# Kernel optimization log

Hardware: AMD Instinct MI355X
Metric: run time of the kernel (lower is better)

Reference implementation:

```python
import jax, jax.numpy as jnp
import numpy as np

B, T, D_IN = 2, 2048, 1024
H, D_HEAD = 16, 64
D_INNER = H * D_HEAD  # 1024
D_OUT = D_HEAD        # out_proj maps d_inner -> d_out


def setup_inputs() -> dict:
    key = jax.random.key(0)
    ks = jax.random.split(key, 6)
    s_in = 1.0 / np.sqrt(D_IN)
    s_inner = 1.0 / np.sqrt(D_INNER)
    return {
        "x": jax.random.normal(ks[0], (B, T, D_IN), dtype=jnp.float32),
        "Wq": jax.random.uniform(ks[1], (D_IN, D_INNER), jnp.float32, -s_in, s_in),
        "Wk": jax.random.uniform(ks[2], (D_IN, D_INNER), jnp.float32, -s_in, s_in),
        "Wv": jax.random.uniform(ks[3], (D_IN, D_INNER), jnp.float32, -s_in, s_in),
        "Wo": jax.random.uniform(ks[4], (D_INNER, D_OUT), jnp.float32, -s_inner, s_inner),
        "bo": jax.random.uniform(ks[5], (D_OUT,), jnp.float32, -s_inner, s_inner),
    }


def reference(x, Wq, Wk, Wv, Wo, bo):
    b, t, _ = x.shape
    # projections -> [b, h, t, d]
    def split_heads(y):
        return y.reshape(b, t, H, D_HEAD).transpose(0, 2, 1, 3)
    q = split_heads(x @ Wq)
    k = split_heads(x @ Wk)
    v = split_heads(x @ Wv)
    scores = jnp.einsum("bhqd,bhkd->bhqk", q, k)
    causal = jnp.triu(jnp.ones((t, t), dtype=bool), k=1)
    scores = jnp.where(causal, -jnp.inf, scores)
    # NOTE: original scales by sqrt(d_out*num_heads), not sqrt(head_dim)
    attn = jax.nn.softmax(scores / np.sqrt(D_INNER), axis=-1)
    y = jnp.einsum("bhqk,bhkd->bhqd", attn, v)
    y = y.transpose(0, 2, 1, 3).reshape(b, t, D_INNER)
    return y @ Wo + bo
```

## Files before the change

### kernel.cpp

```cpp
#include <hip/hip_runtime.h>

typedef __attribute__((ext_vector_type(8))) short short8;
typedef __attribute__((ext_vector_type(4))) float f32x4;
typedef __attribute__((ext_vector_type(8))) unsigned short ushort8v;


__device__ __forceinline__ unsigned short f2bf(float f) {
  union { float f; unsigned int u; } x; x.f = f;
  unsigned int r = x.u + 0x7FFFu + ((x.u >> 16) & 1u);
  return (unsigned short)(r >> 16);
}

__device__ __forceinline__ void gload_lds16(const void* g, void* l) {
  __builtin_amdgcn_global_load_lds(
      (const __attribute__((address_space(1))) void*)g,
      (__attribute__((address_space(3))) void*)l, 16, 0, 0);
}


__global__ __launch_bounds__(256) void prep(
    const float* __restrict__ x,
    const float* __restrict__ Wq, const float* __restrict__ Wk, const float* __restrict__ Wv,
    const float* __restrict__ Wo, const float* __restrict__ bo,
    unsigned short* __restrict__ xb,
    unsigned short* __restrict__ wqt, unsigned short* __restrict__ wkt,
    unsigned short* __restrict__ wvt, unsigned short* __restrict__ wot,
    float* __restrict__ out) {
  __shared__ float tile[32][33];
  int b = blockIdx.x;
  if (b < 4096) {
    int i = (b * 256 + threadIdx.x) * 4;
    float4 f = *(const float4*)(x + i);
    ushort4 o;
    o.x = f2bf(f.x); o.y = f2bf(f.y); o.z = f2bf(f.z); o.w = f2bf(f.w);
    *(ushort4*)(xb + i) = o;
  } else if (b < 7168) {
    int idx = b - 4096;
    int z = idx >> 10, rem = idx & 1023;
    const float* src = (z == 0) ? Wq : (z == 1) ? Wk : Wv;
    unsigned short* dst = (z == 0) ? wqt : (z == 1) ? wkt : wvt;
    int kx = (rem & 31) * 32, ny = (rem >> 5) * 32;
    int tx = threadIdx.x & 31, ty = threadIdx.x >> 5;
    #pragma unroll
    for (int r = 0; r < 32; r += 8)
      tile[ty + r][tx] = src[(size_t)(kx + ty + r) * 1024 + ny + tx];
    __syncthreads();
    #pragma unroll
    for (int r = 0; r < 32; r += 8)
      dst[(size_t)(ny + ty + r) * 1024 + kx + tx] = f2bf(tile[tx][ty + r]);
  } else if (b < 7232) {
    int idx = b - 7168;
    int kx = (idx & 31) * 32, ny = (idx >> 5) * 32;
    int tx = threadIdx.x & 31, ty = threadIdx.x >> 5;
    #pragma unroll
    for (int r = 0; r < 32; r += 8)
      tile[ty + r][tx] = Wo[(size_t)(kx + ty + r) * 64 + ny + tx];
    __syncthreads();
    #pragma unroll
    for (int r = 0; r < 32; r += 8)
      wot[(size_t)(ny + ty + r) * 1024 + kx + tx] = f2bf(tile[tx][ty + r]);
  } else {
    int t = (b - 7232) * 256 + threadIdx.x;
    float4 bi = *(const float4*)(bo + (t & 15) * 4);
    *(float4*)(out + (size_t)t * 4) = bi;
  }
}


__global__ __launch_bounds__(256) void qkv_gemm(
    const unsigned short* __restrict__ Xb,
    const unsigned short* __restrict__ Wqt, const unsigned short* __restrict__ Wkt,
    const unsigned short* __restrict__ Wvt,
    unsigned short* __restrict__ Oq, unsigned short* __restrict__ Ok,
    unsigned short* __restrict__ Ovt) {
  constexpr int Kd = 1024;
  __shared__ __align__(16) unsigned short As[128 * 64];
  __shared__ __align__(16) unsigned short Bs[128 * 64];
  int z = blockIdx.z;
  int m0, n0;
  const unsigned short *Arow, *Brow;
  if (z == 2) {
    m0 = blockIdx.x * 128; n0 = blockIdx.y * 128;
    Arow = Xb; Brow = Wvt;
  } else {
    m0 = blockIdx.y * 128; n0 = blockIdx.x * 128;
    Arow = (z == 0) ? Wqt : Wkt; Brow = Xb;
  }
  int tid = threadIdx.x, lane = tid & 63, wave = tid >> 6;
  int wm = wave >> 1, wn = wave & 1;
  int l15 = lane & 15, quad = lane >> 4;
  int swz = l15 & 7;

  f32x4 acc[4][4] = {};

  for (int k0 = 0; k0 < Kd; k0 += 64) {
    __syncthreads();
    #pragma unroll
    for (int r = 0; r < 4; ++r) {
      int i = tid + 256 * r;
      int row = i >> 3, c8 = i & 7;
      int gc8 = c8 ^ (row & 7);
      gload_lds16(Arow + (size_t)(m0 + row) * Kd + k0 + gc8 * 8, &As[i * 8]);
    }
    #pragma unroll
    for (int r = 0; r < 4; ++r) {
      int i = tid + 256 * r;
      int row = i >> 3, c8 = i & 7;
      int gc8 = c8 ^ (row & 7);
      gload_lds16(Brow + (size_t)(n0 + row) * Kd + k0 + gc8 * 8, &Bs[i * 8]);
    }
    __syncthreads();
    short8 af[4][2], bf[4][2];
    #pragma unroll
    for (int s = 0; s < 2; ++s) {
      #pragma unroll
      for (int i = 0; i < 4; ++i)
        af[i][s] = *(const short8*)&As[(wm * 64 + i * 16 + l15) * 64 + (((s << 2) + quad) ^ swz) * 8];
      #pragma unroll
      for (int j = 0; j < 4; ++j)
        bf[j][s] = *(const short8*)&Bs[(wn * 64 + j * 16 + l15) * 64 + (((s << 2) + quad) ^ swz) * 8];
    }
    #pragma unroll
    for (int s = 0; s < 2; ++s)
      #pragma unroll
      for (int i = 0; i < 4; ++i)
        #pragma unroll
        for (int j = 0; j < 4; ++j)
          acc[i][j] = __builtin_amdgcn_mfma_f32_16x16x32_bf16(af[i][s], bf[j][s], acc[i][j], 0, 0, 0);
  }

  if (z == 2) {
    #pragma unroll
    for (int i = 0; i < 4; ++i) {
      int tbase = m0 + wm * 64 + i * 16 + quad * 4;
      int b = tbase >> 11, tt = tbase & 2047;
      #pragma unroll
      for (int j = 0; j < 4; ++j) {
        int dm = n0 + wn * 64 + j * 16 + l15;
        int h = dm >> 6, d = dm & 63;
        unsigned int u0 = f2bf(acc[i][j][0]), u1 = f2bf(acc[i][j][1]);
        unsigned int u2 = f2bf(acc[i][j][2]), u3 = f2bf(acc[i][j][3]);
        uint2 pk; pk.x = u0 | (u1 << 16); pk.y = u2 | (u3 << 16);
        *(uint2*)(Ovt + (((size_t)(b * 16 + h) * 64 + d) << 11) + tt) = pk;
      }
    }
  } else {
    unsigned short* O = (z == 0) ? Oq : Ok;
    float scale = (z == 0) ? 0.0450842200f : 1.0f;
    #pragma unroll
    for (int i = 0; i < 4; ++i) {
      int dmbase = m0 + wm * 64 + i * 16 + quad * 4;
      int h = dmbase >> 6, d0 = dmbase & 63;
      #pragma unroll
      for (int j = 0; j < 4; ++j) {
        int t = n0 + wn * 64 + j * 16 + l15;
        int b = t >> 11, tt = t & 2047;
        unsigned int u0 = f2bf(acc[i][j][0] * scale), u1 = f2bf(acc[i][j][1] * scale);
        unsigned int u2 = f2bf(acc[i][j][2] * scale), u3 = f2bf(acc[i][j][3] * scale);
        uint2 pk; pk.x = u0 | (u1 << 16); pk.y = u2 | (u3 << 16);
        *(uint2*)(O + (((size_t)(b * 16 + h) * 2048 + tt) << 6) + d0) = pk;
      }
    }
  }
}


__global__ __launch_bounds__(256, 2) void attn10(
    const unsigned short* __restrict__ Qg, const unsigned short* __restrict__ Kg,
    const unsigned short* __restrict__ Vtg, unsigned short* __restrict__ Yg) {
  constexpr int T = 2048;
  __shared__ __align__(16) unsigned short Ks[2][64 * 64];
  __shared__ __align__(16) unsigned short Vs[2][64 * 64];
  __shared__ __align__(16) unsigned short Ps[4][32 * 64];
  int bh = blockIdx.x;
  int by = blockIdx.y;
  int pp = (by < 8) ? by : 23 - by;
  int qtA = pp, qtB = 31 - pp;
  int tid = threadIdx.x, lane = tid & 63, wave = tid >> 6;
  int l15 = lane & 15, quad = lane >> 4;
  int swz = l15 & 7;
  const unsigned short* Qb = Qg + (size_t)bh * T * 64;
  const unsigned short* Kb = Kg + (size_t)bh * T * 64;
  const unsigned short* Vb = Vtg + (size_t)bh * 64 * T;
  int h = bh & 15, b = bh >> 4;
  int qw[2] = {qtA * 64 + wave * 16, qtB * 64 + wave * 16};

  short8 qf[2][2];
  #pragma unroll
  for (int jq = 0; jq < 2; ++jq)
    #pragma unroll
    for (int s = 0; s < 2; ++s)
      qf[jq][s] = *(const short8*)(Qb + (size_t)(qw[jq] + l15) * 64 + quad * 8 + 32 * s);

  f32x4 Oacc[2][4] = {};
  float m_run[2] = {-__builtin_inff(), -__builtin_inff()};
  float l_run[2] = {0.f, 0.f};

  int srow = tid >> 3, sc8 = tid & 7;
  int sdst = srow * 64 + ((sc8 ^ (srow & 7)) * 8);

  ushort8v kpre[2], vpre[2];
  #pragma unroll
  for (int r = 0; r < 2; ++r) {
    kpre[r] = *(const ushort8v*)(Kb + (size_t)(srow + 32 * r) * 64 + sc8 * 8);
    vpre[r] = *(const ushort8v*)(Vb + (size_t)(srow + 32 * r) * T + sc8 * 8);
  }
  *(ushort8v*)&Ks[0][sdst] = kpre[0];
  *(ushort8v*)&Ks[0][sdst + 2048] = kpre[1];
  *(ushort8v*)&Vs[0][sdst] = vpre[0];
  *(ushort8v*)&Vs[0][sdst + 2048] = vpre[1];
  __syncthreads();

  for (int kt = 0; kt <= qtA; ++kt) {
    const unsigned short* Kl = Ks[kt & 1];
    const unsigned short* Vl = Vs[kt & 1];
    unsigned short* Kn = Ks[(kt & 1) ^ 1];
    unsigned short* Vn = Vs[(kt & 1) ^ 1];

    #pragma unroll
    for (int r = 0; r < 2; ++r) {
      kpre[r] = *(const ushort8v*)(Kb + (size_t)((kt + 1) * 64 + srow + 32 * r) * 64 + sc8 * 8);
      vpre[r] = *(const ushort8v*)(Vb + (size_t)(srow + 32 * r) * T + (kt + 1) * 64 + sc8 * 8);
    }

    f32x4 S[4][2] = {};
    __builtin_amdgcn_s_setprio(1);
    #pragma unroll
    for (int s = 0; s < 2; ++s)
      #pragma unroll
      for (int mi = 0; mi < 4; ++mi) {
        short8 kf = *(const short8*)&Kl[(mi * 16 + l15) * 64 + ((quad + 4 * s) ^ swz) * 8];
        #pragma unroll
        for (int jq = 0; jq < 2; ++jq)
          S[mi][jq] = __builtin_amdgcn_mfma_f32_16x16x32_bf16(kf, qf[jq][s], S[mi][jq], 0, 0, 0);
      }
    __builtin_amdgcn_s_setprio(0);

    if (kt == qtA) {
      int ql = wave * 16 + l15;
      #pragma unroll
      for (int mi = 0; mi < 4; ++mi) {
        int tokl = mi * 16 + quad * 4;
        #pragma unroll
        for (int r = 0; r < 4; ++r)
          if (tokl + r > ql) S[mi][0][r] = -__builtin_inff();
      }
    }

    float alpha[2]; bool norescale[2];
    #pragma unroll
    for (int jq = 0; jq < 2; ++jq) {
      float t0 = fmaxf(fmaxf(S[0][jq][0], S[0][jq][1]), fmaxf(S[0][jq][2], S[0][jq][3]));
      float t1 = fmaxf(fmaxf(S[1][jq][0], S[1][jq][1]), fmaxf(S[1][jq][2], S[1][jq][3]));
      float t2 = fmaxf(fmaxf(S[2][jq][0], S[2][jq][1]), fmaxf(S[2][jq][2], S[2][jq][3]));
      float t3 = fmaxf(fmaxf(S[3][jq][0], S[3][jq][1]), fmaxf(S[3][jq][2], S[3][jq][3]));
      float vmax = fmaxf(fmaxf(t0, t1), fmaxf(t2, t3));
      vmax = fmaxf(vmax, __shfl_xor(vmax, 16));
      vmax = fmaxf(vmax, __shfl_xor(vmax, 32));
      float mold = m_run[jq];
      bool defer = __all(vmax - mold <= 8.f) != 0;
      float mnew = defer ? mold : fmaxf(mold, vmax);
      alpha[jq] = defer ? 1.f : __builtin_amdgcn_exp2f(mold - mnew);
      norescale[jq] = defer;
      m_run[jq] = mnew;
      float rs = 0.f;
      #pragma unroll
      for (int mi = 0; mi < 4; ++mi) {
        float p0 = __builtin_amdgcn_exp2f(S[mi][jq][0] - mnew);
        float p1 = __builtin_amdgcn_exp2f(S[mi][jq][1] - mnew);
        float p2 = __builtin_amdgcn_exp2f(S[mi][jq][2] - mnew);
        float p3 = __builtin_amdgcn_exp2f(S[mi][jq][3] - mnew);
        rs += (p0 + p1) + (p2 + p3);
        union { float f; unsigned int u; } a0{p0}, a1{p1}, a2{p2}, a3{p3};
        uint2 pk;
        pk.x = ((a0.u + 0x8000u) >> 16) | ((a1.u + 0x8000u) & 0xFFFF0000u);
        pk.y = ((a2.u + 0x8000u) >> 16) | ((a3.u + 0x8000u) & 0xFFFF0000u);
        int g = (2 * mi + (quad >> 1)) ^ swz;
        *(uint2*)&Ps[wave][(jq * 16 + l15) * 64 + g * 8 + (quad & 1) * 4] = pk;
      }
      rs += __shfl_xor(rs, 16);
      rs += __shfl_xor(rs, 32);
      l_run[jq] = l_run[jq] * alpha[jq] + rs;
    }

    #pragma unroll
    for (int jq = 0; jq < 2; ++jq)
      if (!norescale[jq])
        #pragma unroll
        for (int jd = 0; jd < 4; ++jd)
          #pragma unroll
          for (int r = 0; r < 4; ++r)
            Oacc[jq][jd][r] *= alpha[jq];

    *(ushort8v*)&Kn[sdst] = kpre[0];
    *(ushort8v*)&Kn[sdst + 2048] = kpre[1];
    *(ushort8v*)&Vn[sdst] = vpre[0];
    *(ushort8v*)&Vn[sdst + 2048] = vpre[1];

    __builtin_amdgcn_s_setprio(1);
    #pragma unroll
    for (int s = 0; s < 2; ++s) {
      short8 vfr[4];
      #pragma unroll
      for (int jd = 0; jd < 4; ++jd)
        vfr[jd] = *(const short8*)&Vl[(jd * 16 + l15) * 64 + ((quad + 4 * s) ^ swz) * 8];
      #pragma unroll
      for (int jq = 0; jq < 2; ++jq) {
        short8 pf = *(const short8*)&Ps[wave][(jq * 16 + l15) * 64 + ((quad + 4 * s) ^ swz) * 8];
        #pragma unroll
        for (int jd = 0; jd < 4; ++jd)
          Oacc[jq][jd] = __builtin_amdgcn_mfma_f32_16x16x32_bf16(vfr[jd], pf, Oacc[jq][jd], 0, 0, 0);
      }
    }
    __builtin_amdgcn_s_setprio(0);
    __syncthreads();
  }

  for (int kt = qtA + 1; kt <= qtB; ++kt) {
    const unsigned short* Kl = Ks[kt & 1];
    const unsigned short* Vl = Vs[kt & 1];
    unsigned short* Kn = Ks[(kt & 1) ^ 1];
    unsigned short* Vn = Vs[(kt & 1) ^ 1];

    if (kt < qtB) {
      #pragma unroll
      for (int r = 0; r < 2; ++r) {
        kpre[r] = *(const ushort8v*)(Kb + (size_t)((kt + 1) * 64 + srow + 32 * r) * 64 + sc8 * 8);
        vpre[r] = *(const ushort8v*)(Vb + (size_t)(srow + 32 * r) * T + (kt + 1) * 64 + sc8 * 8);
      }
    }

    f32x4 S[4] = {};
    __builtin_amdgcn_s_setprio(1);
    #pragma unroll
    for (int s = 0; s < 2; ++s)
      #pragma unroll
      for (int mi = 0; mi < 4; ++mi) {
        short8 kf = *(const short8*)&Kl[(mi * 16 + l15) * 64 + ((quad + 4 * s) ^ swz) * 8];
        S[mi] = __builtin_amdgcn_mfma_f32_16x16x32_bf16(kf, qf[1][s], S[mi], 0, 0, 0);
      }
    __builtin_amdgcn_s_setprio(0);

    if (kt == qtB) {
      int ql = wave * 16 + l15;
      #pragma unroll
      for (int mi = 0; mi < 4; ++mi) {
        int tokl = mi * 16 + quad * 4;
        #pragma unroll
        for (int r = 0; r < 4; ++r)
          if (tokl + r > ql) S[mi][r] = -__builtin_inff();
      }
    }

    float t0 = fmaxf(fmaxf(S[0][0], S[0][1]), fmaxf(S[0][2], S[0][3]));
    float t1 = fmaxf(fmaxf(S[1][0], S[1][1]), fmaxf(S[1][2], S[1][3]));
    float t2 = fmaxf(fmaxf(S[2][0], S[2][1]), fmaxf(S[2][2], S[2][3]));
    float t3 = fmaxf(fmaxf(S[3][0], S[3][1]), fmaxf(S[3][2], S[3][3]));
    float vmax = fmaxf(fmaxf(t0, t1), fmaxf(t2, t3));
    vmax = fmaxf(vmax, __shfl_xor(vmax, 16));
    vmax = fmaxf(vmax, __shfl_xor(vmax, 32));
    float mold = m_run[1];
    bool defer = __all(vmax - mold <= 8.f) != 0;
    float mnew = defer ? mold : fmaxf(mold, vmax);
    float alpha = defer ? 1.f : __builtin_amdgcn_exp2f(mold - mnew);
    m_run[1] = mnew;
    float rs = 0.f;
    #pragma unroll
    for (int mi = 0; mi < 4; ++mi) {
      float p0 = __builtin_amdgcn_exp2f(S[mi][0] - mnew);
      float p1 = __builtin_amdgcn_exp2f(S[mi][1] - mnew);
      float p2 = __builtin_amdgcn_exp2f(S[mi][2] - mnew);
      float p3 = __builtin_amdgcn_exp2f(S[mi][3] - mnew);
      rs += (p0 + p1) + (p2 + p3);
      union { float f; unsigned int u; } a0{p0}, a1{p1}, a2{p2}, a3{p3};
      uint2 pk;
      pk.x = ((a0.u + 0x8000u) >> 16) | ((a1.u + 0x8000u) & 0xFFFF0000u);
      pk.y = ((a2.u + 0x8000u) >> 16) | ((a3.u + 0x8000u) & 0xFFFF0000u);
      int g = (2 * mi + (quad >> 1)) ^ swz;
      *(uint2*)&Ps[wave][(16 + l15) * 64 + g * 8 + (quad & 1) * 4] = pk;
    }
    rs += __shfl_xor(rs, 16);
    rs += __shfl_xor(rs, 32);
    l_run[1] = l_run[1] * alpha + rs;

    if (!defer)
      #pragma unroll
      for (int jd = 0; jd < 4; ++jd)
        #pragma unroll
        for (int r = 0; r < 4; ++r)
          Oacc[1][jd][r] *= alpha;

    if (kt < qtB) {
      *(ushort8v*)&Kn[sdst] = kpre[0];
      *(ushort8v*)&Kn[sdst + 2048] = kpre[1];
      *(ushort8v*)&Vn[sdst] = vpre[0];
      *(ushort8v*)&Vn[sdst + 2048] = vpre[1];
    }

    __builtin_amdgcn_s_setprio(1);
    #pragma unroll
    for (int s = 0; s < 2; ++s) {
      short8 pf = *(const short8*)&Ps[wave][(16 + l15) * 64 + ((quad + 4 * s) ^ swz) * 8];
      #pragma unroll
      for (int jd = 0; jd < 4; ++jd) {
        short8 vfr = *(const short8*)&Vl[(jd * 16 + l15) * 64 + ((quad + 4 * s) ^ swz) * 8];
        Oacc[1][jd] = __builtin_amdgcn_mfma_f32_16x16x32_bf16(vfr, pf, Oacc[1][jd], 0, 0, 0);
      }
    }
    __builtin_amdgcn_s_setprio(0);
    __syncthreads();
  }

  #pragma unroll
  for (int jq = 0; jq < 2; ++jq) {
    float linv = 1.f / l_run[jq];
    int q = qw[jq] + l15;
    size_t row = (size_t)(b * 2048 + q) * 1024 + h * 64 + quad * 4;
    #pragma unroll
    for (int jd = 0; jd < 4; ++jd) {
      unsigned int u0 = f2bf(Oacc[jq][jd][0] * linv), u1 = f2bf(Oacc[jq][jd][1] * linv);
      unsigned int u2 = f2bf(Oacc[jq][jd][2] * linv), u3 = f2bf(Oacc[jq][jd][3] * linv);
      uint2 pk; pk.x = u0 | (u1 << 16); pk.y = u2 | (u3 << 16);
      *(uint2*)(Yg + row + jd * 16) = pk;
    }
  }
}


__global__ __launch_bounds__(256) void oproj(
    const unsigned short* __restrict__ Y, const unsigned short* __restrict__ Wot,
    float* __restrict__ out) {
  __shared__ __align__(16) unsigned short As[64 * 32];
  __shared__ __align__(16) unsigned short Bs[64 * 32];
  int m0 = blockIdx.x * 64;
  int kbase = blockIdx.y * 256;
  int tid = threadIdx.x, lane = tid & 63, wave = tid >> 6;
  int l15 = lane & 15, quad = lane >> 4;
  f32x4 acc[4] = {};
  for (int k0 = kbase; k0 < kbase + 256; k0 += 32) {
    __syncthreads();
    {
      int row = tid >> 2, c8 = (tid & 3) * 8;
      gload_lds16(Y + (size_t)(m0 + row) * 1024 + k0 + c8, &As[tid * 8]);
      gload_lds16(Wot + (size_t)row * 1024 + k0 + c8, &Bs[tid * 8]);
    }
    __syncthreads();
    short8 af = *(const short8*)&As[(wave * 16 + l15) * 32 + quad * 8];
    #pragma unroll
    for (int j = 0; j < 4; ++j) {
      short8 bf = *(const short8*)&Bs[(j * 16 + l15) * 32 + quad * 8];
      acc[j] = __builtin_amdgcn_mfma_f32_16x16x32_bf16(af, bf, acc[j], 0, 0, 0);
    }
  }
  #pragma unroll
  for (int j = 0; j < 4; ++j) {
    int n = j * 16 + l15;
    #pragma unroll
    for (int r = 0; r < 4; ++r) {
      int m = m0 + wave * 16 + quad * 4 + r;
      atomicAdd(&out[(size_t)m * 64 + n], acc[j][r]);
    }
  }
}


extern "C" void kernel_launch(void* const* d_in, const int* in_sizes, int n_in,
                              void* d_out, int out_size, void* d_ws, size_t ws_size,
                              hipStream_t stream) {
  const float* x  = (const float*)d_in[0];
  const float* Wq = (const float*)d_in[1];
  const float* Wk = (const float*)d_in[2];
  const float* Wv = (const float*)d_in[3];
  const float* Wo = (const float*)d_in[4];
  const float* bo = (const float*)d_in[5];
  float* out = (float*)d_out;
  char* ws = (char*)d_ws;

  unsigned short* xb  = (unsigned short*)(ws);
  unsigned short* wqt = (unsigned short*)(ws + (8ull << 20));
  unsigned short* wkt = (unsigned short*)(ws + (10ull << 20));
  unsigned short* wvt = (unsigned short*)(ws + (12ull << 20));
  unsigned short* wot = (unsigned short*)(ws + (14ull << 20));
  unsigned short* q   = (unsigned short*)(ws + (15ull << 20));
  unsigned short* k   = (unsigned short*)(ws + (23ull << 20));
  unsigned short* vt  = (unsigned short*)(ws + (31ull << 20));
  unsigned short* y   = (unsigned short*)(ws + (39ull << 20));

  prep<<<7488, 256, 0, stream>>>(x, Wq, Wk, Wv, Wo, bo, xb, wqt, wkt, wvt, wot, out);
  qkv_gemm<<<dim3(32, 8, 3), 256, 0, stream>>>(xb, wqt, wkt, wvt, q, k, vt);
  attn10<<<dim3(32, 16), 256, 0, stream>>>(q, k, vt, y);
  oproj<<<dim3(64, 4), 256, 0, stream>>>(y, wot, out);
}
```

Baseline: 163.0 us.

## Split paired causal query tiles into one tile per block for higher occupancy

The attention kernel no longer gives each block two query tiles (a short and a long one paired for causal balance). Each block now handles a single 64-row query tile, so the grid doubles to 32x32 blocks. Blocks are ordered so short and long tiles interleave, and the P staging buffer is halved. This cuts registers and shared memory per block so launch bounds can request 4 blocks per CU instead of 2, and the final barrier is skipped. The cost is that K/V tiles for the low-index key ranges are loaded by more blocks, and per-block work becomes uneven, which now relies on the scheduler to balance it.

```diff
diff --git a/kernel.cpp b/kernel.cpp
--- a/kernel.cpp
+++ b/kernel.cpp
@@ -165,17 +165,17 @@
 }
 
 
-__global__ __launch_bounds__(256, 2) void attn10(
+__global__ __launch_bounds__(256, 4) void attn11(
     const unsigned short* __restrict__ Qg, const unsigned short* __restrict__ Kg,
     const unsigned short* __restrict__ Vtg, unsigned short* __restrict__ Yg) {
   constexpr int T = 2048;
   __shared__ __align__(16) unsigned short Ks[2][64 * 64];
   __shared__ __align__(16) unsigned short Vs[2][64 * 64];
-  __shared__ __align__(16) unsigned short Ps[4][32 * 64];
+  __shared__ __align__(16) unsigned short Ps[4][16 * 64];
   int bh = blockIdx.x;
   int by = blockIdx.y;
-  int pp = (by < 8) ? by : 23 - by;
-  int qtA = pp, qtB = 31 - pp;
+  int g = by >> 3, w8 = by & 7;
+  int qt = (g == 0) ? w8 : (g == 1) ? (15 - w8) : (g == 2) ? (16 + w8) : (31 - w8);
   int tid = threadIdx.x, lane = tid & 63, wave = tid >> 6;
   int l15 = lane & 15, quad = lane >> 4;
   int swz = l15 & 7;
@@ -183,18 +183,16 @@
   const unsigned short* Kb = Kg + (size_t)bh * T * 64;
   const unsigned short* Vb = Vtg + (size_t)bh * 64 * T;
   int h = bh & 15, b = bh >> 4;
-  int qw[2] = {qtA * 64 + wave * 16, qtB * 64 + wave * 16};
-
-  short8 qf[2][2];
+  int qw = qt * 64 + wave * 16;
+
+  short8 qf[2];
   #pragma unroll
-  for (int jq = 0; jq < 2; ++jq)
-    #pragma unroll
-    for (int s = 0; s < 2; ++s)
-      qf[jq][s] = *(const short8*)(Qb + (size_t)(qw[jq] + l15) * 64 + quad * 8 + 32 * s);
-
-  f32x4 Oacc[2][4] = {};
-  float m_run[2] = {-__builtin_inff(), -__builtin_inff()};
-  float l_run[2] = {0.f, 0.f};
+  for (int s = 0; s < 2; ++s)
+    qf[s] = *(const short8*)(Qb + (size_t)(qw + l15) * 64 + quad * 8 + 32 * s);
+
+  f32x4 Oacc[4] = {};
+  float m_run = -__builtin_inff();
+  float l_run = 0.f;
 
   int srow = tid >> 3, sc8 = tid & 7;
   int sdst = srow * 64 + ((sc8 ^ (srow & 7)) * 8);
@@ -211,118 +209,13 @@
   *(ushort8v*)&Vs[0][sdst + 2048] = vpre[1];
   __syncthreads();
 
-  for (int kt = 0; kt <= qtA; ++kt) {
+  for (int kt = 0; kt <= qt; ++kt) {
     const unsigned short* Kl = Ks[kt & 1];
     const unsigned short* Vl = Vs[kt & 1];
     unsigned short* Kn = Ks[(kt & 1) ^ 1];
     unsigned short* Vn = Vs[(kt & 1) ^ 1];
 
-    #pragma unroll
-    for (int r = 0; r < 2; ++r) {
-      kpre[r] = *(const ushort8v*)(Kb + (size_t)((kt + 1) * 64 + srow + 32 * r) * 64 + sc8 * 8);
-      vpre[r] = *(const ushort8v*)(Vb + (size_t)(srow + 32 * r) * T + (kt + 1) * 64 + sc8 * 8);
-    }
-
-    f32x4 S[4][2] = {};
-    __builtin_amdgcn_s_setprio(1);
-    #pragma unroll
-    for (int s = 0; s < 2; ++s)
-      #pragma unroll
-      for (int mi = 0; mi < 4; ++mi) {
-        short8 kf = *(const short8*)&Kl[(mi * 16 + l15) * 64 + ((quad + 4 * s) ^ swz) * 8];
-        #pragma unroll
-        for (int jq = 0; jq < 2; ++jq)
-          S[mi][jq] = __builtin_amdgcn_mfma_f32_16x16x32_bf16(kf, qf[jq][s], S[mi][jq], 0, 0, 0);
-      }
-    __builtin_amdgcn_s_setprio(0);
-
-    if (kt == qtA) {
-      int ql = wave * 16 + l15;
-      #pragma unroll
-      for (int mi = 0; mi < 4; ++mi) {
-        int tokl = mi * 16 + quad * 4;
-        #pragma unroll
-        for (int r = 0; r < 4; ++r)
-          if (tokl + r > ql) S[mi][0][r] = -__builtin_inff();
-      }
-    }
-
-    float alpha[2]; bool norescale[2];
-    #pragma unroll
-    for (int jq = 0; jq < 2; ++jq) {
-      float t0 = fmaxf(fmaxf(S[0][jq][0], S[0][jq][1]), fmaxf(S[0][jq][2], S[0][jq][3]));
-      float t1 = fmaxf(fmaxf(S[1][jq][0], S[1][jq][1]), fmaxf(S[1][jq][2], S[1][jq][3]));
-      float t2 = fmaxf(fmaxf(S[2][jq][0], S[2][jq][1]), fmaxf(S[2][jq][2], S[2][jq][3]));
-      float t3 = fmaxf(fmaxf(S[3][jq][0], S[3][jq][1]), fmaxf(S[3][jq][2], S[3][jq][3]));
-      float vmax = fmaxf(fmaxf(t0, t1), fmaxf(t2, t3));
-      vmax = fmaxf(vmax, __shfl_xor(vmax, 16));
-      vmax = fmaxf(vmax, __shfl_xor(vmax, 32));
-      float mold = m_run[jq];
-      bool defer = __all(vmax - mold <= 8.f) != 0;
-      float mnew = defer ? mold : fmaxf(mold, vmax);
-      alpha[jq] = defer ? 1.f : __builtin_amdgcn_exp2f(mold - mnew);
-      norescale[jq] = defer;
-      m_run[jq] = mnew;
-      float rs = 0.f;
-      #pragma unroll
-      for (int mi = 0; mi < 4; ++mi) {
-        float p0 = __builtin_amdgcn_exp2f(S[mi][jq][0] - mnew);
-        float p1 = __builtin_amdgcn_exp2f(S[mi][jq][1] - mnew);
-        float p2 = __builtin_amdgcn_exp2f(S[mi][jq][2] - mnew);
-        float p3 = __builtin_amdgcn_exp2f(S[mi][jq][3] - mnew);
-        rs += (p0 + p1) + (p2 + p3);
-        union { float f; unsigned int u; } a0{p0}, a1{p1}, a2{p2}, a3{p3};
-        uint2 pk;
-        pk.x = ((a0.u + 0x8000u) >> 16) | ((a1.u + 0x8000u) & 0xFFFF0000u);
-        pk.y = ((a2.u + 0x8000u) >> 16) | ((a3.u + 0x8000u) & 0xFFFF0000u);
-        int g = (2 * mi + (quad >> 1)) ^ swz;
-        *(uint2*)&Ps[wave][(jq * 16 + l15) * 64 + g * 8 + (quad & 1) * 4] = pk;
-      }
-      rs += __shfl_xor(rs, 16);
-      rs += __shfl_xor(rs, 32);
-      l_run[jq] = l_run[jq] * alpha[jq] + rs;
-    }
-
-    #pragma unroll
-    for (int jq = 0; jq < 2; ++jq)
-      if (!norescale[jq])
-        #pragma unroll
-        for (int jd = 0; jd < 4; ++jd)
-          #pragma unroll
-          for (int r = 0; r < 4; ++r)
-            Oacc[jq][jd][r] *= alpha[jq];
-
-    *(ushort8v*)&Kn[sdst] = kpre[0];
-    *(ushort8v*)&Kn[sdst + 2048] = kpre[1];
-    *(ushort8v*)&Vn[sdst] = vpre[0];
-    *(ushort8v*)&Vn[sdst + 2048] = vpre[1];
-
-    __builtin_amdgcn_s_setprio(1);
-    #pragma unroll
-    for (int s = 0; s < 2; ++s) {
-      short8 vfr[4];
-      #pragma unroll
-      for (int jd = 0; jd < 4; ++jd)
-        vfr[jd] = *(const short8*)&Vl[(jd * 16 + l15) * 64 + ((quad + 4 * s) ^ swz) * 8];
-      #pragma unroll
-      for (int jq = 0; jq < 2; ++jq) {
-        short8 pf = *(const short8*)&Ps[wave][(jq * 16 + l15) * 64 + ((quad + 4 * s) ^ swz) * 8];
-        #pragma unroll
-        for (int jd = 0; jd < 4; ++jd)
-          Oacc[jq][jd] = __builtin_amdgcn_mfma_f32_16x16x32_bf16(vfr[jd], pf, Oacc[jq][jd], 0, 0, 0);
-      }
-    }
-    __builtin_amdgcn_s_setprio(0);
-    __syncthreads();
-  }
-
-  for (int kt = qtA + 1; kt <= qtB; ++kt) {
-    const unsigned short* Kl = Ks[kt & 1];
-    const unsigned short* Vl = Vs[kt & 1];
-    unsigned short* Kn = Ks[(kt & 1) ^ 1];
-    unsigned short* Vn = Vs[(kt & 1) ^ 1];
-
-    if (kt < qtB) {
+    if (kt < qt) {
       #pragma unroll
       for (int r = 0; r < 2; ++r) {
         kpre[r] = *(const ushort8v*)(Kb + (size_t)((kt + 1) * 64 + srow + 32 * r) * 64 + sc8 * 8);
@@ -337,11 +230,11 @@
       #pragma unroll
       for (int mi = 0; mi < 4; ++mi) {
         short8 kf = *(const short8*)&Kl[(mi * 16 + l15) * 64 + ((quad + 4 * s) ^ swz) * 8];
-        S[mi] = __builtin_amdgcn_mfma_f32_16x16x32_bf16(kf, qf[1][s], S[mi], 0, 0, 0);
+        S[mi] = __builtin_amdgcn_mfma_f32_16x16x32_bf16(kf, qf[s], S[mi], 0, 0, 0);
       }
     __builtin_amdgcn_s_setprio(0);
 
-    if (kt == qtB) {
+    if (kt == qt) {
       int ql = wave * 16 + l15;
       #pragma unroll
       for (int mi = 0; mi < 4; ++mi) {
@@ -359,11 +252,11 @@
     float vmax = fmaxf(fmaxf(t0, t1), fmaxf(t2, t3));
     vmax = fmaxf(vmax, __shfl_xor(vmax, 16));
     vmax = fmaxf(vmax, __shfl_xor(vmax, 32));
-    float mold = m_run[1];
+    float mold = m_run;
     bool defer = __all(vmax - mold <= 8.f) != 0;
     float mnew = defer ? mold : fmaxf(mold, vmax);
     float alpha = defer ? 1.f : __builtin_amdgcn_exp2f(mold - mnew);
-    m_run[1] = mnew;
+    m_run = mnew;
     float rs = 0.f;
     #pragma unroll
     for (int mi = 0; mi < 4; ++mi) {
@@ -376,21 +269,21 @@
       uint2 pk;
       pk.x = ((a0.u + 0x8000u) >> 16) | ((a1.u + 0x8000u) & 0xFFFF0000u);
       pk.y = ((a2.u + 0x8000u) >> 16) | ((a3.u + 0x8000u) & 0xFFFF0000u);
-      int g = (2 * mi + (quad >> 1)) ^ swz;
-      *(uint2*)&Ps[wave][(16 + l15) * 64 + g * 8 + (quad & 1) * 4] = pk;
+      int gg = (2 * mi + (quad >> 1)) ^ swz;
+      *(uint2*)&Ps[wave][l15 * 64 + gg * 8 + (quad & 1) * 4] = pk;
     }
     rs += __shfl_xor(rs, 16);
     rs += __shfl_xor(rs, 32);
-    l_run[1] = l_run[1] * alpha + rs;
+    l_run = l_run * alpha + rs;
 
     if (!defer)
       #pragma unroll
       for (int jd = 0; jd < 4; ++jd)
         #pragma unroll
         for (int r = 0; r < 4; ++r)
-          Oacc[1][jd][r] *= alpha;
-
-    if (kt < qtB) {
+          Oacc[jd][r] *= alpha;
+
+    if (kt < qt) {
       *(ushort8v*)&Kn[sdst] = kpre[0];
       *(ushort8v*)&Kn[sdst + 2048] = kpre[1];
       *(ushort8v*)&Vn[sdst] = vpre[0];
@@ -400,26 +293,25 @@
     __builtin_amdgcn_s_setprio(1);
     #pragma unroll
     for (int s = 0; s < 2; ++s) {
-      short8 pf = *(const short8*)&Ps[wave][(16 + l15) * 64 + ((quad + 4 * s) ^ swz) * 8];
+      short8 pf = *(const short8*)&Ps[wave][l15 * 64 + ((quad + 4 * s) ^ swz) * 8];
       #pragma unroll
       for (int jd = 0; jd < 4; ++jd) {
         short8 vfr = *(const short8*)&Vl[(jd * 16 + l15) * 64 + ((quad + 4 * s) ^ swz) * 8];
-        Oacc[1][jd] = __builtin_amdgcn_mfma_f32_16x16x32_bf16(vfr, pf, Oacc[1][jd], 0, 0, 0);
+        Oacc[jd] = __builtin_amdgcn_mfma_f32_16x16x32_bf16(vfr, pf, Oacc[jd], 0, 0, 0);
       }
     }
     __builtin_amdgcn_s_setprio(0);
-    __syncthreads();
-  }
-
-  #pragma unroll
-  for (int jq = 0; jq < 2; ++jq) {
-    float linv = 1.f / l_run[jq];
-    int q = qw[jq] + l15;
+    if (kt < qt) __syncthreads();
+  }
+
+  {
+    float linv = 1.f / l_run;
+    int q = qw + l15;
     size_t row = (size_t)(b * 2048 + q) * 1024 + h * 64 + quad * 4;
     #pragma unroll
     for (int jd = 0; jd < 4; ++jd) {
-      unsigned int u0 = f2bf(Oacc[jq][jd][0] * linv), u1 = f2bf(Oacc[jq][jd][1] * linv);
-      unsigned int u2 = f2bf(Oacc[jq][jd][2] * linv), u3 = f2bf(Oacc[jq][jd][3] * linv);
+      unsigned int u0 = f2bf(Oacc[jd][0] * linv), u1 = f2bf(Oacc[jd][1] * linv);
+      unsigned int u2 = f2bf(Oacc[jd][2] * linv), u3 = f2bf(Oacc[jd][3] * linv);
       uint2 pk; pk.x = u0 | (u1 << 16); pk.y = u2 | (u3 << 16);
       *(uint2*)(Yg + row + jd * 16) = pk;
     }
@@ -488,6 +380,6 @@
 
   prep<<<7488, 256, 0, stream>>>(x, Wq, Wk, Wv, Wo, bo, xb, wqt, wkt, wvt, wot, out);
   qkv_gemm<<<dim3(32, 8, 3), 256, 0, stream>>>(xb, wqt, wkt, wvt, q, k, vt);
-  attn10<<<dim3(32, 16), 256, 0, stream>>>(q, k, vt, y);
+  attn11<<<dim3(32, 32), 256, 0, stream>>>(q, k, vt, y);
   oproj<<<dim3(64, 4), 256, 0, stream>>>(y, wot, out);
 }
```

New measurement: 159.0 us. 2.4% less time.
